# Performance work log

Hardware: AMD Instinct MI355X
Metric: run time of the kernel (lower is better)

The kernel has to match this reference:

```python
import jax, jax.numpy as jnp
import numpy as np

B, N, E = 16, 512, 6144          # graphs, sites/graph, edges/graph
D = 256                          # embed_dimension
RBF_DIM = 128
M = 6                            # num_messages
MAXZ = 84                        # max_atomic_num
INIT_MAX_DIST, INIT_GAP = 7.0, 30.0


def setup_inputs() -> dict:
    key = jax.random.key(0)
    ks = jax.random.split(key, 20)
    s = 0.02
    inp = {
        "site_class": jax.random.randint(ks[0], (B, N), 0, MAXZ, dtype=jnp.int64),
        "distance": jax.random.uniform(ks[1], (B, E), dtype=jnp.float32) * INIT_MAX_DIST,
        "connectivity": jax.random.randint(ks[2], (B, E, 2), 0, N, dtype=jnp.int64),
        # learned parameters
        "atom_emb": jax.random.normal(ks[3], (MAXZ, D), jnp.float32) * s,
        "mean_emb": jnp.zeros((MAXZ, 1), jnp.float32),  # Constant(output_bias=0.0)
        "centers": jnp.arange(RBF_DIM, dtype=jnp.float32) * (INIT_MAX_DIST / RBF_DIM),
        "gap": jnp.float32(INIT_GAP),
        "bond_W": jax.random.normal(ks[4], (RBF_DIM, D), jnp.float32) * s,
        "bond_b": jnp.zeros((D,), jnp.float32),
        "offset_W": jax.random.normal(ks[5], (D, 1), jnp.float32) * 1e-6,
        "offset_b": jnp.zeros((1,), jnp.float32),
        # per-message EdgeUpdate ConcatDense: Dense(2D, relu) -> Dense(D), input 3D
        "edge_W1": jax.random.normal(ks[6], (M, 3 * D, 2 * D), jnp.float32) * s,
        "edge_b1": jnp.zeros((M, 2 * D), jnp.float32),
        "edge_W2": jax.random.normal(ks[7], (M, 2 * D, D), jnp.float32) * s,
        "edge_b2": jnp.zeros((M, D), jnp.float32),
        # per-message NodeUpdate ConcatDense: input 2D
        "node_W1": jax.random.normal(ks[8], (M, 2 * D, 2 * D), jnp.float32) * s,
        "node_b1": jnp.zeros((M, 2 * D), jnp.float32),
        "node_W2": jax.random.normal(ks[9], (M, 2 * D, D), jnp.float32) * s,
        "node_b2": jnp.zeros((M, D), jnp.float32),
    }
    return inp


def _gather(x, idx):
    # x: [B, N, D], idx: [B, E] -> [B, E, D]
    return x[jnp.arange(x.shape[0])[:, None], idx]


def reference(site_class, distance, connectivity,
              atom_emb, mean_emb, centers, gap, bond_W, bond_b,
              offset_W, offset_b,
              edge_W1, edge_b1, edge_W2, edge_b2,
              node_W1, node_b1, node_W2, node_b2):
    atom_mask = site_class != 0                     # [B, N] (Embedding mask_zero)
    bond_mask = distance != 0.0                     # [B, E] (RBFExpansion mask)

    atom_state = atom_emb[site_class]               # [B, N, D]
    atom_mean = mean_emb[site_class]                # [B, N, 1]

    # RBF expansion: exp(-gap * (d - centers)^2), masked distances -> 1.0
    d = distance[..., None]
    d = jnp.where(d != 0.0, d, 1.0)
    rbf = jnp.exp(-((d - centers) ** 2) * gap)      # [B, E, RBF_DIM]
    bond_state = rbf @ bond_W + bond_b              # [B, E, D]

    bidx = jnp.arange(site_class.shape[0])[:, None]
    idx0 = connectivity[..., 0]                     # scatter target
    idx1 = connectivity[..., 1]                     # message source

    n_msg = edge_W1.shape[0]
    for i in range(n_msg):
        # EdgeUpdate: concat(bond, src_atom, tgt_atom) -> Dense(2D, relu) -> Dense(D)
        src = _gather(atom_state, idx1)
        tgt = _gather(atom_state, idx0)
        h = jnp.concatenate([bond_state, src, tgt], axis=-1)      # [B, E, 3D]
        h = jax.nn.relu(h @ edge_W1[i] + edge_b1[i])
        h = h @ edge_W2[i] + edge_b2[i]
        h = jnp.where(bond_mask[..., None], h, 0.0)
        bond_state = bond_state + h

        # NodeUpdate: concat(src_atom, bond) -> MLP -> segment-sum onto idx0
        src = _gather(atom_state, idx1)
        m = jnp.concatenate([src, bond_state], axis=-1)           # [B, E, 2D]
        m = jax.nn.relu(m @ node_W1[i] + node_b1[i])
        m = m @ node_W2[i] + node_b2[i]
        new_atom = jnp.zeros_like(atom_state).at[bidx, idx0].add(m)
        new_atom = jnp.where(atom_mask[..., None], new_atom, 0.0)
        atom_state = atom_state + new_atom

    atom_mean = atom_mean + (atom_state @ offset_W + offset_b)   # [B, N, 1]

    # masked global average pooling over sites
    mask_f = atom_mask[..., None].astype(atom_mean.dtype)
    pooled = jnp.sum(atom_mean * mask_f, axis=1) / jnp.sum(mask_f, axis=1)
    return pooled  # [B, 1]
```

## Files before the change

### kernel.cpp

```cpp
#include <hip/hip_runtime.h>
#include <hip/hip_bf16.h>
#include <stdint.h>
#include <stddef.h>

#define Bb 16
#define Nn 512
#define Ee 6144
#define Dd 256
#define ROWS (Bb * Ee)

typedef short bf16x8 __attribute__((ext_vector_type(8)));
typedef float f32x4 __attribute__((ext_vector_type(4)));

__device__ __forceinline__ unsigned short f2bf(float f) {
  union { float f; unsigned u; } v; v.f = f;
  return (unsigned short)((v.u + 0x7fffu + ((v.u >> 16) & 1u)) >> 16);
}
__device__ __forceinline__ float bf2f(unsigned short h) {
  union { unsigned u; float f; } v; v.u = ((unsigned)h) << 16;
  return v.f;
}

__device__ __forceinline__ void gload16(const void* g, void* l) {
  __builtin_amdgcn_global_load_lds(
      (const __attribute__((address_space(1))) void*)g,
      (__attribute__((address_space(3))) void*)l, 16, 0, 0);
}

__global__ void transpose_w(const float* __restrict__ in, unsigned short* __restrict__ out,
                            int K, int Ncol) {
  __shared__ float tile[32][33];
  const float* inb = in + (size_t)blockIdx.z * K * Ncol;
  unsigned short* outb = out + (size_t)blockIdx.z * K * Ncol;
  int bk = blockIdx.x * 32, bn = blockIdx.y * 32;
  int tx = threadIdx.x, ty = threadIdx.y;
#pragma unroll
  for (int i = 0; i < 32; i += 8)
    tile[ty + i][tx] = inb[(size_t)(bk + ty + i) * Ncol + (bn + tx)];
  __syncthreads();
#pragma unroll
  for (int i = 0; i < 32; i += 8)
    outb[(size_t)(bn + ty + i) * K + (bk + tx)] = f2bf(tile[tx][ty + i]);
}

__global__ void atom_init(const int* __restrict__ cls, const float* __restrict__ emb,
                          float* __restrict__ atom, unsigned short* __restrict__ atomBf) {
  int s_ = blockIdx.x, d = threadIdx.x;
  size_t o = (size_t)s_ * Dd + d;
  float v = emb[(size_t)cls[s_] * Dd + d];
  atom[o] = v;
  atomBf[o] = f2bf(v);
}

__global__ void atom_fix(const int* __restrict__ cls, const float* __restrict__ emb,
                         float* __restrict__ atom, unsigned short* __restrict__ atomBf) {
  int s_ = blockIdx.x, d = threadIdx.x;
  size_t o = (size_t)s_ * Dd + d;
  float v = (cls[s_] == 0) ? emb[d] : atom[o];
  atom[o] = v;
  atomBf[o] = f2bf(v);
}

__global__ __launch_bounds__(256, 2) void gemm_rbf(
    const unsigned short* __restrict__ Wt, const float* __restrict__ bias,
    const float* __restrict__ dist, const float* __restrict__ centers,
    const float* __restrict__ gapP, unsigned short* __restrict__ bondHi,
    unsigned short* __restrict__ bondLo) {
  __shared__ __align__(16) unsigned short lA[128 * 64];
  __shared__ __align__(16) unsigned short lB[128 * 64];
  const int t = threadIdx.x;
  const int bm = blockIdx.x * 128, bn = blockIdx.y * 128;
  const int srow = t & 127, skc = (t >> 7) * 32;
  const int m = bm + srow;
  float dval = dist[m]; if (dval == 0.f) dval = 1.f;
  float gapv = *gapP;
  const unsigned short* pBt = Wt + (size_t)(bn + srow) * 128 + skc;
  const int wid = t >> 6, lane = t & 63;
  const int wm = (wid & 1) * 64, wn = (wid >> 1) * 64;
  const int fr = lane & 15, fk0 = (lane >> 4) * 8;
  f32x4 acc[4][4] = {};
  for (int k0 = 0; k0 < 128; k0 += 64) {
    union __align__(16) { unsigned short us[32]; bf16x8 v[4]; } ab, bb;
#pragma unroll
    for (int j = 0; j < 32; j++) {
      float x = dval - centers[k0 + skc + j];
      ab.us[j] = f2bf(__expf(-gapv * x * x));
    }
    const bf16x8* s = (const bf16x8*)(pBt + k0);
#pragma unroll
    for (int c = 0; c < 4; c++) bb.v[c] = s[c];
    __syncthreads();
#pragma unroll
    for (int c = 0; c < 4; c++) {
      int byteo = (skc + c * 8) * 2;
      int swz = byteo ^ ((srow & 7) << 4);
      *(bf16x8*)((char*)lA + srow * 128 + swz) = ab.v[c];
      *(bf16x8*)((char*)lB + srow * 128 + swz) = bb.v[c];
    }
    __syncthreads();
#pragma unroll
    for (int kk = 0; kk < 64; kk += 32) {
      bf16x8 af[4], bfq[4];
#pragma unroll
      for (int f = 0; f < 4; f++) {
        int r = wm + f * 16 + fr;
        af[f] = *(const bf16x8*)((const char*)lA + r * 128 + (((kk + fk0) * 2) ^ ((r & 7) << 4)));
        int cq = wn + f * 16 + fr;
        bfq[f] = *(const bf16x8*)((const char*)lB + cq * 128 + (((kk + fk0) * 2) ^ ((cq & 7) << 4)));
      }
#pragma unroll
      for (int i = 0; i < 4; i++)
#pragma unroll
        for (int j = 0; j < 4; j++)
          acc[i][j] = __builtin_amdgcn_mfma_f32_16x16x32_bf16(af[i], bfq[j], acc[i][j], 0, 0, 0);
    }
  }
#pragma unroll
  for (int i = 0; i < 4; i++)
#pragma unroll
    for (int j = 0; j < 4; j++) {
      int gcol = bn + wn + j * 16 + fr;
      float bvv = bias[gcol];
#pragma unroll
      for (int v = 0; v < 4; v++) {
        int grow = bm + wm + i * 16 + (lane >> 4) * 4 + v;
        float val = acc[i][j][v] + bvv;
        size_t o = (size_t)grow * Dd + gcol;
        unsigned short hi = f2bf(val);
        bondHi[o] = hi;
        bondLo[o] = f2bf(val - bf2f(hi));
      }
    }
}

struct GP {
  const unsigned short* Wt;
  const float* bias;
  const unsigned short* bondHi;
  unsigned short* bondLo;
  const unsigned short* atomBf;
  const unsigned short* h1;
  const int* conn;
  const float* dist;
  unsigned short* outH1;
  unsigned short* outBondHi;
  float* atomMaster;
};

#define A_EDGE1 0
#define A_NODE1 1
#define A_H1    2
#define EP_H1RELU 0
#define EP_EDGE2  1
#define EP_NODE2  2

template <int K, int NC, int AL, int EP>
__global__ __launch_bounds__(512, 4) void gemm128(GP p) {
  __shared__ __align__(16) char lds[65536];
  constexpr int BOFF = 32768;
  const int t = threadIdx.x;
  const int w = t >> 6, l = t & 63;
  constexpr int NT = NC / 128;

  const int nwg = gridDim.x;
  const int q8 = nwg >> 3;
  const int sb = (blockIdx.x & 7) * q8 + (blockIdx.x >> 3);
  const int bn = (sb % NT) * 128;
  const int bm = (sb / NT) * 128;

  const char* pA0[2]; const char* pA1[2]; const char* pA2[2]; const char* pB[2];
#pragma unroll
  for (int i = 0; i < 2; i++) {
    int r = (w * 2 + i) * 8 + (l >> 3);
    int swz = (((l & 7) ^ (r & 7)) << 4);
    if (AL == A_H1) {
      pA0[i] = (const char*)p.h1 + (size_t)(bm + r) * (K * 2) + swz;
      pA1[i] = pA0[i]; pA2[i] = pA0[i];
    } else {
      int gr = bm + r;
      int b = gr / Ee;
      int i0 = p.conn[2 * gr], i1 = p.conn[2 * gr + 1];
      const char* bondRow = (const char*)p.bondHi + (size_t)gr * 512 + swz;
      const char* srcRow  = (const char*)p.atomBf + ((size_t)b * Nn + i1) * 512 + swz;
      const char* tgtRow  = (const char*)p.atomBf + ((size_t)b * Nn + i0) * 512 + swz;
      if (AL == A_EDGE1) { pA0[i] = bondRow; pA1[i] = srcRow; pA2[i] = tgtRow; }
      else               { pA0[i] = srcRow;  pA1[i] = bondRow; pA2[i] = bondRow; }
    }
    pB[i] = (const char*)p.Wt + (size_t)(bn + r) * (K * 2) + swz;
  }

  const int fr = l & 15;
  const int q4 = l >> 4;
  const int wm = (w >> 2) * 64;
  const int wn = (w & 3) * 32;

  f32x4 acc[4][2] = {};

  auto stage = [&](int pb, int k0) {
#pragma unroll
    for (int i = 0; i < 2; i++) {
      const char* src;
      if (AL == A_H1)         src = pA0[i] + k0 * 2;
      else if (AL == A_EDGE1) { int s = k0 >> 8; src = (s == 0 ? pA0[i] : (s == 1 ? pA1[i] : pA2[i])) + (k0 & 255) * 2; }
      else                    src = (k0 < 256 ? pA0[i] : pA1[i]) + (k0 & 255) * 2;
      gload16(src, lds + pb * 16384 + (w * 2 + i) * 1024);
      gload16(pB[i] + k0 * 2, lds + BOFF + pb * 16384 + (w * 2 + i) * 1024);
    }
  };

  auto compute = [&](int pb) {
#pragma unroll
    for (int kk = 0; kk < 2; kk++) {
      const int ck = kk * 4 + q4;
      bf16x8 av[4], bv[2];
#pragma unroll
      for (int f = 0; f < 4; f++) {
        int r = wm + f * 16 + fr;
        av[f] = *(const bf16x8*)(lds + pb * 16384 + r * 128 + ((ck ^ (r & 7)) << 4));
      }
#pragma unroll
      for (int n = 0; n < 2; n++) {
        int rq = wn + n * 16 + fr;
        bv[n] = *(const bf16x8*)(lds + BOFF + pb * 16384 + rq * 128 + ((ck ^ (rq & 7)) << 4));
      }
#pragma unroll
      for (int f = 0; f < 4; f++)
#pragma unroll
        for (int n = 0; n < 2; n++)
          acc[f][n] = __builtin_amdgcn_mfma_f32_16x16x32_bf16(av[f], bv[n], acc[f][n], 0, 0, 0);
    }
  };

  constexpr int nT = K / 64;
  stage(0, 0);
  __syncthreads();
  for (int tt = 0; tt < nT; tt++) {
    int pb = tt & 1;
    if (tt + 1 < nT) stage(pb ^ 1, (tt + 1) * 64);
    compute(pb);
    __syncthreads();
  }

  float bias2[2];
#pragma unroll
  for (int n = 0; n < 2; n++) bias2[n] = p.bias[bn + wn + n * 16 + fr];

#pragma unroll
  for (int f = 0; f < 4; f++) {
#pragma unroll
    for (int v = 0; v < 4; v++) {
      int grow = bm + wm + f * 16 + q4 * 4 + v;
      if (EP == EP_H1RELU) {
#pragma unroll
        for (int n = 0; n < 2; n++) {
          int gcol = bn + wn + n * 16 + fr;
          float val = acc[f][n][v] + bias2[n];
          p.outH1[(size_t)grow * 512 + gcol] = f2bf(fmaxf(val, 0.f));
        }
      } else if (EP == EP_EDGE2) {
        if (p.dist[grow] != 0.f) {
#pragma unroll
          for (int n = 0; n < 2; n++) {
            int gcol = bn + wn + n * 16 + fr;
            size_t o = (size_t)grow * Dd + gcol;
            float cur = bf2f(p.bondHi[o]) + bf2f(p.bondLo[o]);
            float nv = cur + acc[f][n][v] + bias2[n];
            unsigned short hi = f2bf(nv);
            p.outBondHi[o] = hi;
            p.bondLo[o] = f2bf(nv - bf2f(hi));
          }
        }
      } else {
        int b = grow / Ee;
        int tg = p.conn[2 * grow];
        float* dst = p.atomMaster + ((size_t)b * Nn + tg) * Dd;
#pragma unroll
        for (int n = 0; n < 2; n++) {
          int gcol = bn + wn + n * 16 + fr;
          atomicAdd(dst + gcol, acc[f][n][v] + bias2[n]);
        }
      }
    }
  }
}

__global__ void pool_k(const float* __restrict__ atom, const int* __restrict__ cls,
                       const float* __restrict__ meanEmb, const float* __restrict__ oW,
                       const float* __restrict__ ob, float* __restrict__ out) {
  __shared__ float w[Dd];
  __shared__ float red[256];
  __shared__ float redc[256];
  int b = blockIdx.x, t = threadIdx.x;
  w[t] = oW[t];
  __syncthreads();
  float sum = 0.f, cnt = 0.f;
  for (int n = t; n < Nn; n += 256) {
    int site = b * Nn + n;
    int c = cls[site];
    const float* a = atom + (size_t)site * Dd;
    float dot = 0.f;
    for (int d = 0; d < Dd; d++) dot += a[d] * w[d];
    if (c != 0) { sum += meanEmb[c] + dot + ob[0]; cnt += 1.f; }
  }
  red[t] = sum; redc[t] = cnt;
  __syncthreads();
  for (int s = 128; s > 0; s >>= 1) {
    if (t < s) { red[t] += red[t + s]; redc[t] += redc[t + s]; }
    __syncthreads();
  }
  if (t == 0) out[b] = red[0] / redc[0];
}

extern "C" void kernel_launch(void* const* d_in, const int* in_sizes, int n_in,
                              void* d_out, int out_size, void* d_ws, size_t ws_size,
                              hipStream_t stream) {
  const int* site_class = (const int*)d_in[0];
  const float* distance = (const float*)d_in[1];
  const int* conn       = (const int*)d_in[2];
  const float* atom_emb = (const float*)d_in[3];
  const float* mean_emb = (const float*)d_in[4];
  const float* centers  = (const float*)d_in[5];
  const float* gapP     = (const float*)d_in[6];
  const float* bond_W   = (const float*)d_in[7];
  const float* bond_b   = (const float*)d_in[8];
  const float* offset_W = (const float*)d_in[9];
  const float* offset_b = (const float*)d_in[10];
  const float* edge_W1  = (const float*)d_in[11];
  const float* edge_b1  = (const float*)d_in[12];
  const float* edge_W2  = (const float*)d_in[13];
  const float* edge_b2  = (const float*)d_in[14];
  const float* node_W1  = (const float*)d_in[15];
  const float* node_b1  = (const float*)d_in[16];
  const float* node_W2  = (const float*)d_in[17];
  const float* node_b2  = (const float*)d_in[18];

  char* ws = (char*)d_ws;
  float* atom            = (float*)(ws + 0);
  unsigned short* atomBf = (unsigned short*)(ws + 8388608);
  unsigned short* bondHi = (unsigned short*)(ws + 12582912);
  unsigned short* bondLo = (unsigned short*)(ws + 62914560);
  unsigned short* h1     = (unsigned short*)(ws + 113246208);
  unsigned short* bWT    = (unsigned short*)(ws + 213909504);
  unsigned short* eW1T   = (unsigned short*)(ws + 213975040);
  unsigned short* eW2T   = (unsigned short*)(ws + 218693632);
  unsigned short* nW1T   = (unsigned short*)(ws + 220266496);
  unsigned short* nW2T   = (unsigned short*)(ws + 223412224);

  dim3 tb(32, 8);
  transpose_w<<<dim3(4, 8, 1), tb, 0, stream>>>(bond_W, bWT, 128, 256);
  transpose_w<<<dim3(24, 16, 6), tb, 0, stream>>>(edge_W1, eW1T, 768, 512);
  transpose_w<<<dim3(16, 8, 6), tb, 0, stream>>>(edge_W2, eW2T, 512, 256);
  transpose_w<<<dim3(16, 16, 6), tb, 0, stream>>>(node_W1, nW1T, 512, 512);
  transpose_w<<<dim3(16, 8, 6), tb, 0, stream>>>(node_W2, nW2T, 512, 256);

  atom_init<<<Bb * Nn, 256, 0, stream>>>(site_class, atom_emb, atom, atomBf);
  gemm_rbf<<<dim3(768, 2), 256, 0, stream>>>(bWT, bond_b, distance, centers, gapP, bondHi, bondLo);

  GP base{};
  base.conn = conn; base.dist = distance;
  base.bondHi = bondHi; base.bondLo = bondLo; base.atomBf = atomBf; base.h1 = h1;
  base.outH1 = h1; base.outBondHi = bondHi; base.atomMaster = atom;

  for (int i = 0; i < 6; i++) {
    {
      GP q = base;
      q.Wt = eW1T + (size_t)i * 512 * 768; q.bias = edge_b1 + i * 512;
      gemm128<768, 512, A_EDGE1, EP_H1RELU><<<3072, 512, 0, stream>>>(q);
    }
    {
      GP q = base;
      q.Wt = eW2T + (size_t)i * 256 * 512; q.bias = edge_b2 + i * 256;
      gemm128<512, 256, A_H1, EP_EDGE2><<<1536, 512, 0, stream>>>(q);
    }
    {
      GP q = base;
      q.Wt = nW1T + (size_t)i * 512 * 512; q.bias = node_b1 + i * 512;
      gemm128<512, 512, A_NODE1, EP_H1RELU><<<3072, 512, 0, stream>>>(q);
    }
    {
      GP q = base;
      q.Wt = nW2T + (size_t)i * 256 * 512; q.bias = node_b2 + i * 256;
      gemm128<512, 256, A_H1, EP_NODE2><<<1536, 512, 0, stream>>>(q);
    }
    atom_fix<<<Bb * Nn, 256, 0, stream>>>(site_class, atom_emb, atom, atomBf);
  }

  pool_k<<<Bb, 256, 0, stream>>>(atom, site_class, mean_emb, offset_W, offset_b, (float*)d_out);
}
```

Before: 1.953 ms.

## Enlarge GEMM tiles to 256x256 with deeper prefetch pipeline

```diff
diff --git a/kernel.cpp b/kernel.cpp
--- a/kernel.cpp
+++ b/kernel.cpp
@@ -155,116 +155,132 @@
 #define EP_NODE2  2
 
 template <int K, int NC, int AL, int EP>
-__global__ __launch_bounds__(512, 4) void gemm128(GP p) {
-  __shared__ __align__(16) char lds[65536];
-  constexpr int BOFF = 32768;
+__global__ __launch_bounds__(512, 2) void gemm256(GP p) {
+  __shared__ __align__(16) char lds[131072];
   const int t = threadIdx.x;
   const int w = t >> 6, l = t & 63;
-  constexpr int NT = NC / 128;
+  constexpr int NT = NC / 256;
 
   const int nwg = gridDim.x;
   const int q8 = nwg >> 3;
   const int sb = (blockIdx.x & 7) * q8 + (blockIdx.x >> 3);
-  const int bn = (sb % NT) * 128;
-  const int bm = (sb / NT) * 128;
-
-  const char* pA0[2]; const char* pA1[2]; const char* pA2[2]; const char* pB[2];
-#pragma unroll
-  for (int i = 0; i < 2; i++) {
-    int r = (w * 2 + i) * 8 + (l >> 3);
-    int swz = (((l & 7) ^ (r & 7)) << 4);
+  const int bn = (sb % NT) * 256;
+  const int bm = (sb / NT) * 256;
+
+  const unsigned swz = (unsigned)(((l & 7) ^ (l >> 3)) << 4);
+
+  unsigned offA0[4], offA1[4], offA2[4], offB[4];
+#pragma unroll
+  for (int i = 0; i < 4; i++) {
+    int rA = i * 64 + w * 8 + (l >> 3);
     if (AL == A_H1) {
-      pA0[i] = (const char*)p.h1 + (size_t)(bm + r) * (K * 2) + swz;
-      pA1[i] = pA0[i]; pA2[i] = pA0[i];
+      offA0[i] = (unsigned)(bm + rA) * (K * 2) + swz;
+      offA1[i] = offA0[i]; offA2[i] = offA0[i];
     } else {
-      int gr = bm + r;
+      int gr = bm + rA;
       int b = gr / Ee;
       int i0 = p.conn[2 * gr], i1 = p.conn[2 * gr + 1];
-      const char* bondRow = (const char*)p.bondHi + (size_t)gr * 512 + swz;
-      const char* srcRow  = (const char*)p.atomBf + ((size_t)b * Nn + i1) * 512 + swz;
-      const char* tgtRow  = (const char*)p.atomBf + ((size_t)b * Nn + i0) * 512 + swz;
-      if (AL == A_EDGE1) { pA0[i] = bondRow; pA1[i] = srcRow; pA2[i] = tgtRow; }
-      else               { pA0[i] = srcRow;  pA1[i] = bondRow; pA2[i] = bondRow; }
-    }
-    pB[i] = (const char*)p.Wt + (size_t)(bn + r) * (K * 2) + swz;
+      unsigned bondOff = (unsigned)gr * 512u + swz;
+      unsigned srcOff  = (unsigned)(b * Nn + i1) * 512u + swz;
+      unsigned tgtOff  = (unsigned)(b * Nn + i0) * 512u + swz;
+      if (AL == A_EDGE1) { offA0[i] = bondOff; offA1[i] = srcOff; offA2[i] = tgtOff; }
+      else               { offA0[i] = srcOff;  offA1[i] = bondOff; offA2[i] = bondOff; }
+    }
+    offB[i] = (unsigned)(bn + rA) * (K * 2) + swz;
   }
 
   const int fr = l & 15;
   const int q4 = l >> 4;
-  const int wm = (w >> 2) * 64;
-  const int wn = (w & 3) * 32;
-
-  f32x4 acc[4][2] = {};
-
-  auto stage = [&](int pb, int k0) {
-#pragma unroll
-    for (int i = 0; i < 2; i++) {
+  const int wm = (w >> 2) * 128;
+  const int wn = (w & 3) * 64;
+
+  f32x4 acc[8][4] = {};
+
+  auto stage = [&](int buf, int k0) {
+#pragma unroll
+    for (int i = 0; i < 4; i++) {
       const char* src;
-      if (AL == A_H1)         src = pA0[i] + k0 * 2;
-      else if (AL == A_EDGE1) { int s = k0 >> 8; src = (s == 0 ? pA0[i] : (s == 1 ? pA1[i] : pA2[i])) + (k0 & 255) * 2; }
-      else                    src = (k0 < 256 ? pA0[i] : pA1[i]) + (k0 & 255) * 2;
-      gload16(src, lds + pb * 16384 + (w * 2 + i) * 1024);
-      gload16(pB[i] + k0 * 2, lds + BOFF + pb * 16384 + (w * 2 + i) * 1024);
+      if (AL == A_H1) {
+        src = (const char*)p.h1 + (offA0[i] + (unsigned)k0 * 2);
+      } else if (AL == A_EDGE1) {
+        int s = k0 >> 8;
+        src = (s == 0 ? (const char*)p.bondHi + offA0[i]
+                      : (const char*)p.atomBf + (s == 1 ? offA1[i] : offA2[i]))
+              + (k0 & 255) * 2;
+      } else {
+        src = (k0 < 256 ? (const char*)p.atomBf + offA0[i]
+                        : (const char*)p.bondHi + offA1[i])
+              + (k0 & 255) * 2;
+      }
+      gload16(src, lds + buf * 32768 + i * 8192 + w * 1024);
+      gload16((const char*)p.Wt + offB[i] + (unsigned)k0 * 2,
+              lds + 65536 + buf * 32768 + i * 8192 + w * 1024);
     }
   };
 
-  auto compute = [&](int pb) {
+  auto compute = [&](int buf) {
 #pragma unroll
     for (int kk = 0; kk < 2; kk++) {
       const int ck = kk * 4 + q4;
-      bf16x8 av[4], bv[2];
-#pragma unroll
-      for (int f = 0; f < 4; f++) {
+      bf16x8 av[8], bv[4];
+#pragma unroll
+      for (int f = 0; f < 8; f++) {
         int r = wm + f * 16 + fr;
-        av[f] = *(const bf16x8*)(lds + pb * 16384 + r * 128 + ((ck ^ (r & 7)) << 4));
-      }
-#pragma unroll
-      for (int n = 0; n < 2; n++) {
+        av[f] = *(const bf16x8*)(lds + buf * 32768 + r * 128 + ((ck ^ (r & 7)) << 4));
+      }
+#pragma unroll
+      for (int n = 0; n < 4; n++) {
         int rq = wn + n * 16 + fr;
-        bv[n] = *(const bf16x8*)(lds + BOFF + pb * 16384 + rq * 128 + ((ck ^ (rq & 7)) << 4));
-      }
-#pragma unroll
-      for (int f = 0; f < 4; f++)
-#pragma unroll
-        for (int n = 0; n < 2; n++)
+        bv[n] = *(const bf16x8*)(lds + 65536 + buf * 32768 + rq * 128 + ((ck ^ (rq & 7)) << 4));
+      }
+      __builtin_amdgcn_s_setprio(1);
+#pragma unroll
+      for (int f = 0; f < 8; f++)
+#pragma unroll
+        for (int n = 0; n < 4; n++)
           acc[f][n] = __builtin_amdgcn_mfma_f32_16x16x32_bf16(av[f], bv[n], acc[f][n], 0, 0, 0);
+      __builtin_amdgcn_s_setprio(0);
     }
   };
 
   constexpr int nT = K / 64;
   stage(0, 0);
-  __syncthreads();
+  stage(1, 64);
+
   for (int tt = 0; tt < nT; tt++) {
-    int pb = tt & 1;
-    if (tt + 1 < nT) stage(pb ^ 1, (tt + 1) * 64);
-    compute(pb);
-    __syncthreads();
-  }
-
-  float bias2[2];
-#pragma unroll
-  for (int n = 0; n < 2; n++) bias2[n] = p.bias[bn + wn + n * 16 + fr];
-
-#pragma unroll
-  for (int f = 0; f < 4; f++) {
+    asm volatile("s_waitcnt vmcnt(8)" ::: "memory");
+    __builtin_amdgcn_s_barrier();
+    __builtin_amdgcn_sched_barrier(0);
+    compute(tt & 1);
+    __builtin_amdgcn_s_barrier();
+    __builtin_amdgcn_sched_barrier(0);
+    if (tt + 2 < nT) stage(tt & 1, (tt + 2) * 64);
+  }
+
+  float bias4[4];
+#pragma unroll
+  for (int n = 0; n < 4; n++) bias4[n] = p.bias[bn + wn + n * 16 + fr];
+
+#pragma unroll
+  for (int f = 0; f < 8; f++) {
 #pragma unroll
     for (int v = 0; v < 4; v++) {
       int grow = bm + wm + f * 16 + q4 * 4 + v;
       if (EP == EP_H1RELU) {
 #pragma unroll
-        for (int n = 0; n < 2; n++) {
+        for (int n = 0; n < 4; n++) {
           int gcol = bn + wn + n * 16 + fr;
-          float val = acc[f][n][v] + bias2[n];
+          float val = acc[f][n][v] + bias4[n];
           p.outH1[(size_t)grow * 512 + gcol] = f2bf(fmaxf(val, 0.f));
         }
       } else if (EP == EP_EDGE2) {
         if (p.dist[grow] != 0.f) {
 #pragma unroll
-          for (int n = 0; n < 2; n++) {
+          for (int n = 0; n < 4; n++) {
             int gcol = bn + wn + n * 16 + fr;
             size_t o = (size_t)grow * Dd + gcol;
             float cur = bf2f(p.bondHi[o]) + bf2f(p.bondLo[o]);
-            float nv = cur + acc[f][n][v] + bias2[n];
+            float nv = cur + acc[f][n][v] + bias4[n];
             unsigned short hi = f2bf(nv);
             p.outBondHi[o] = hi;
             p.bondLo[o] = f2bf(nv - bf2f(hi));
@@ -275,9 +291,9 @@
         int tg = p.conn[2 * grow];
         float* dst = p.atomMaster + ((size_t)b * Nn + tg) * Dd;
 #pragma unroll
-        for (int n = 0; n < 2; n++) {
+        for (int n = 0; n < 4; n++) {
           int gcol = bn + wn + n * 16 + fr;
-          atomicAdd(dst + gcol, acc[f][n][v] + bias2[n]);
+          atomicAdd(dst + gcol, acc[f][n][v] + bias4[n]);
         }
       }
     }
@@ -365,22 +381,22 @@
     {
       GP q = base;
       q.Wt = eW1T + (size_t)i * 512 * 768; q.bias = edge_b1 + i * 512;
-      gemm128<768, 512, A_EDGE1, EP_H1RELU><<<3072, 512, 0, stream>>>(q);
+      gemm256<768, 512, A_EDGE1, EP_H1RELU><<<768, 512, 0, stream>>>(q);
     }
     {
       GP q = base;
       q.Wt = eW2T + (size_t)i * 256 * 512; q.bias = edge_b2 + i * 256;
-      gemm128<512, 256, A_H1, EP_EDGE2><<<1536, 512, 0, stream>>>(q);
+      gemm256<512, 256, A_H1, EP_EDGE2><<<384, 512, 0, stream>>>(q);
     }
     {
       GP q = base;
       q.Wt = nW1T + (size_t)i * 512 * 512; q.bias = node_b1 + i * 512;
-      gemm128<512, 512, A_NODE1, EP_H1RELU><<<3072, 512, 0, stream>>>(q);
+      gemm256<512, 512, A_NODE1, EP_H1RELU><<<768, 512, 0, stream>>>(q);
     }
     {
       GP q = base;
       q.Wt = nW2T + (size_t)i * 256 * 512; q.bias = node_b2 + i * 256;
-      gemm128<512, 256, A_H1, EP_NODE2><<<1536, 512, 0, stream>>>(q);
+      gemm256<512, 256, A_H1, EP_NODE2><<<384, 512, 0, stream>>>(q);
     }
     atom_fix<<<Bb * Nn, 256, 0, stream>>>(site_class, atom_emb, atom, atomBf);
   }
```

Result: slower. 2.343 ms (+20.0%).

## Precompute per-atom projections of gathered inputs instead of per-edge GEMM over concat

Applied to the files above, without the earlier changes.

```diff
diff --git a/kernel.cpp b/kernel.cpp
--- a/kernel.cpp
+++ b/kernel.cpp
@@ -8,6 +8,7 @@
 #define Ee 6144
 #define Dd 256
 #define ROWS (Bb * Ee)
+#define HALF (ROWS / 2)
 
 typedef short bf16x8 __attribute__((ext_vector_type(8)));
 typedef float f32x4 __attribute__((ext_vector_type(4)));
@@ -134,27 +135,29 @@
 }
 
 struct GP {
+  const unsigned short* A;
   const unsigned short* Wt;
   const float* bias;
+  const int* conn;
+  const float* dist;
   const unsigned short* bondHi;
   unsigned short* bondLo;
-  const unsigned short* atomBf;
-  const unsigned short* h1;
-  const int* conn;
-  const float* dist;
+  unsigned short* outBondHi;
+  const float* tab0;
+  const float* tab1;
   unsigned short* outH1;
-  unsigned short* outBondHi;
+  float* outTab;
   float* atomMaster;
+  int rowBase;
 };
 
-#define A_EDGE1 0
-#define A_NODE1 1
-#define A_H1    2
-#define EP_H1RELU 0
-#define EP_EDGE2  1
-#define EP_NODE2  2
-
-template <int K, int NC, int AL, int EP>
+#define EP_TAB    0
+#define EP_H1E    1
+#define EP_H1N    2
+#define EP_EDGE2  3
+#define EP_NODE2  4
+
+template <int K, int WS, int NC, int EP>
 __global__ __launch_bounds__(512, 4) void gemm128(GP p) {
   __shared__ __align__(16) char lds[65536];
   constexpr int BOFF = 32768;
@@ -168,25 +171,13 @@
   const int bn = (sb % NT) * 128;
   const int bm = (sb / NT) * 128;
 
-  const char* pA0[2]; const char* pA1[2]; const char* pA2[2]; const char* pB[2];
+  const char* pA[2]; const char* pB[2];
 #pragma unroll
   for (int i = 0; i < 2; i++) {
     int r = (w * 2 + i) * 8 + (l >> 3);
     int swz = (((l & 7) ^ (r & 7)) << 4);
-    if (AL == A_H1) {
-      pA0[i] = (const char*)p.h1 + (size_t)(bm + r) * (K * 2) + swz;
-      pA1[i] = pA0[i]; pA2[i] = pA0[i];
-    } else {
-      int gr = bm + r;
-      int b = gr / Ee;
-      int i0 = p.conn[2 * gr], i1 = p.conn[2 * gr + 1];
-      const char* bondRow = (const char*)p.bondHi + (size_t)gr * 512 + swz;
-      const char* srcRow  = (const char*)p.atomBf + ((size_t)b * Nn + i1) * 512 + swz;
-      const char* tgtRow  = (const char*)p.atomBf + ((size_t)b * Nn + i0) * 512 + swz;
-      if (AL == A_EDGE1) { pA0[i] = bondRow; pA1[i] = srcRow; pA2[i] = tgtRow; }
-      else               { pA0[i] = srcRow;  pA1[i] = bondRow; pA2[i] = bondRow; }
-    }
-    pB[i] = (const char*)p.Wt + (size_t)(bn + r) * (K * 2) + swz;
+    pA[i] = (const char*)p.A  + (size_t)(bm + r) * (K * 2) + swz;
+    pB[i] = (const char*)p.Wt + (size_t)(bn + r) * (WS * 2) + swz;
   }
 
   const int fr = l & 15;
@@ -199,11 +190,7 @@
   auto stage = [&](int pb, int k0) {
 #pragma unroll
     for (int i = 0; i < 2; i++) {
-      const char* src;
-      if (AL == A_H1)         src = pA0[i] + k0 * 2;
-      else if (AL == A_EDGE1) { int s = k0 >> 8; src = (s == 0 ? pA0[i] : (s == 1 ? pA1[i] : pA2[i])) + (k0 & 255) * 2; }
-      else                    src = (k0 < 256 ? pA0[i] : pA1[i]) + (k0 & 255) * 2;
-      gload16(src, lds + pb * 16384 + (w * 2 + i) * 1024);
+      gload16(pA[i] + k0 * 2, lds + pb * 16384 + (w * 2 + i) * 1024);
       gload16(pB[i] + k0 * 2, lds + BOFF + pb * 16384 + (w * 2 + i) * 1024);
     }
   };
@@ -242,27 +229,42 @@
   }
 
   float bias2[2];
-#pragma unroll
-  for (int n = 0; n < 2; n++) bias2[n] = p.bias[bn + wn + n * 16 + fr];
+  if (EP != EP_TAB) {
+#pragma unroll
+    for (int n = 0; n < 2; n++) bias2[n] = p.bias[bn + wn + n * 16 + fr];
+  }
 
 #pragma unroll
   for (int f = 0; f < 4; f++) {
 #pragma unroll
     for (int v = 0; v < 4; v++) {
-      int grow = bm + wm + f * 16 + q4 * 4 + v;
-      if (EP == EP_H1RELU) {
+      int lrow = bm + wm + f * 16 + q4 * 4 + v;
+      if (EP == EP_TAB) {
 #pragma unroll
         for (int n = 0; n < 2; n++) {
           int gcol = bn + wn + n * 16 + fr;
-          float val = acc[f][n][v] + bias2[n];
-          p.outH1[(size_t)grow * 512 + gcol] = f2bf(fmaxf(val, 0.f));
+          p.outTab[(size_t)lrow * 512 + gcol] = acc[f][n][v];
+        }
+      } else if (EP == EP_H1E || EP == EP_H1N) {
+        int gr = p.rowBase + lrow;
+        int b = gr / Ee;
+        int i0 = p.conn[2 * gr], i1 = p.conn[2 * gr + 1];
+        const float* sR = p.tab0 + ((size_t)(b * Nn + i1)) * 512;
+        const float* tR = (EP == EP_H1E) ? (p.tab1 + ((size_t)(b * Nn + i0)) * 512) : nullptr;
+#pragma unroll
+        for (int n = 0; n < 2; n++) {
+          int gcol = bn + wn + n * 16 + fr;
+          float val = acc[f][n][v] + bias2[n] + sR[gcol];
+          if (EP == EP_H1E) val += tR[gcol];
+          p.outH1[(size_t)lrow * 512 + gcol] = f2bf(fmaxf(val, 0.f));
         }
       } else if (EP == EP_EDGE2) {
-        if (p.dist[grow] != 0.f) {
+        int gr = p.rowBase + lrow;
+        if (p.dist[gr] != 0.f) {
 #pragma unroll
           for (int n = 0; n < 2; n++) {
             int gcol = bn + wn + n * 16 + fr;
-            size_t o = (size_t)grow * Dd + gcol;
+            size_t o = (size_t)gr * Dd + gcol;
             float cur = bf2f(p.bondHi[o]) + bf2f(p.bondLo[o]);
             float nv = cur + acc[f][n][v] + bias2[n];
             unsigned short hi = f2bf(nv);
@@ -271,8 +273,9 @@
           }
         }
       } else {
-        int b = grow / Ee;
-        int tg = p.conn[2 * grow];
+        int gr = p.rowBase + lrow;
+        int b = gr / Ee;
+        int tg = p.conn[2 * gr];
         float* dst = p.atomMaster + ((size_t)b * Nn + tg) * Dd;
 #pragma unroll
         for (int n = 0; n < 2; n++) {
@@ -340,11 +343,13 @@
   unsigned short* bondHi = (unsigned short*)(ws + 12582912);
   unsigned short* bondLo = (unsigned short*)(ws + 62914560);
   unsigned short* h1     = (unsigned short*)(ws + 113246208);
-  unsigned short* bWT    = (unsigned short*)(ws + 213909504);
-  unsigned short* eW1T   = (unsigned short*)(ws + 213975040);
-  unsigned short* eW2T   = (unsigned short*)(ws + 218693632);
-  unsigned short* nW1T   = (unsigned short*)(ws + 220266496);
-  unsigned short* nW2T   = (unsigned short*)(ws + 223412224);
+  float* tabS            = (float*)(ws + 163577856);
+  float* tabT            = (float*)(ws + 180355072);
+  unsigned short* bWT    = (unsigned short*)(ws + 197132288);
+  unsigned short* eW1T   = (unsigned short*)(ws + 197197824);
+  unsigned short* eW2T   = (unsigned short*)(ws + 201916416);
+  unsigned short* nW1T   = (unsigned short*)(ws + 203489280);
+  unsigned short* nW2T   = (unsigned short*)(ws + 206635008);
 
   dim3 tb(32, 8);
   transpose_w<<<dim3(4, 8, 1), tb, 0, stream>>>(bond_W, bWT, 128, 256);
@@ -358,29 +363,38 @@
 
   GP base{};
   base.conn = conn; base.dist = distance;
-  base.bondHi = bondHi; base.bondLo = bondLo; base.atomBf = atomBf; base.h1 = h1;
-  base.outH1 = h1; base.outBondHi = bondHi; base.atomMaster = atom;
+  base.bondHi = bondHi; base.bondLo = bondLo; base.outBondHi = bondHi;
+  base.tab0 = tabS; base.tab1 = tabT;
+  base.outH1 = h1; base.atomMaster = atom;
 
   for (int i = 0; i < 6; i++) {
+    const unsigned short* eW1i = eW1T + (size_t)i * 512 * 768;
+    const unsigned short* nW1i = nW1T + (size_t)i * 512 * 512;
     {
-      GP q = base;
-      q.Wt = eW1T + (size_t)i * 512 * 768; q.bias = edge_b1 + i * 512;
-      gemm128<768, 512, A_EDGE1, EP_H1RELU><<<3072, 512, 0, stream>>>(q);
+      GP q = base; q.A = atomBf; q.Wt = eW1i + 256; q.outTab = tabS; q.rowBase = 0;
+      gemm128<256, 768, 512, EP_TAB><<<256, 512, 0, stream>>>(q);
+      GP r = base; r.A = atomBf; r.Wt = eW1i + 512; r.outTab = tabT; r.rowBase = 0;
+      gemm128<256, 768, 512, EP_TAB><<<256, 512, 0, stream>>>(r);
+    }
+    for (int h = 0; h < 2; h++) {
+      GP q = base; q.A = bondHi + (size_t)h * HALF * Dd; q.Wt = eW1i;
+      q.bias = edge_b1 + i * 512; q.rowBase = h * HALF;
+      gemm128<256, 768, 512, EP_H1E><<<1536, 512, 0, stream>>>(q);
+      GP r = base; r.A = h1; r.Wt = eW2T + (size_t)i * 256 * 512;
+      r.bias = edge_b2 + i * 256; r.rowBase = h * HALF;
+      gemm128<512, 512, 256, EP_EDGE2><<<768, 512, 0, stream>>>(r);
     }
     {
-      GP q = base;
-      q.Wt = eW2T + (size_t)i * 256 * 512; q.bias = edge_b2 + i * 256;
-      gemm128<512, 256, A_H1, EP_EDGE2><<<1536, 512, 0, stream>>>(q);
-    }
-    {
-      GP q = base;
-      q.Wt = nW1T + (size_t)i * 512 * 512; q.bias = node_b1 + i * 512;
-      gemm128<512, 512, A_NODE1, EP_H1RELU><<<3072, 512, 0, stream>>>(q);
-    }
-    {
-      GP q = base;
-      q.Wt = nW2T + (size_t)i * 256 * 512; q.bias = node_b2 + i * 256;
-      gemm128<512, 256, A_H1, EP_NODE2><<<1536, 512, 0, stream>>>(q);
+      GP q = base; q.A = atomBf; q.Wt = nW1i; q.outTab = tabS; q.rowBase = 0;
+      gemm128<256, 512, 512, EP_TAB><<<256, 512, 0, stream>>>(q);
+    }
+    for (int h = 0; h < 2; h++) {
+      GP q = base; q.A = bondHi + (size_t)h * HALF * Dd; q.Wt = nW1i + 256;
+      q.bias = node_b1 + i * 512; q.rowBase = h * HALF;
+      gemm128<256, 512, 512, EP_H1N><<<1536, 512, 0, stream>>>(q);
+      GP r = base; r.A = h1; r.Wt = nW2T + (size_t)i * 256 * 512;
+      r.bias = node_b2 + i * 256; r.rowBase = h * HALF;
+      gemm128<512, 512, 256, EP_NODE2><<<768, 512, 0, stream>>>(r);
     }
     atom_fix<<<Bb * Nn, 256, 0, stream>>>(site_class, atom_emb, atom, atomBf);
   }
```

Result: slower. 2.127 ms (+8.9%).
